# Performance work log

Hardware: AMD Instinct MI355X
Metric: run time of the kernel (lower is better)

The kernel has to match this reference:

```python
import jax, jax.numpy as jnp
import numpy as np

B, NQ, NV = 4, 16384, 16384
DIM, FRAMES = 64, 4
D = DIM * FRAMES            # embed_dims = 256
HEADS, POINTS, LEVELS = 8, 4, 1
HD = D // HEADS             # head_dim = 32
HL, WL = 128, 128           # single-level feature map, HL*WL == NV
EPS = 1e-6


def setup_inputs() -> dict:
    key = jax.random.key(0)
    ks = jax.random.split(key, 14)
    inp = {
        "query": jax.random.normal(ks[0], (B, NQ, D), jnp.float32),
        "feat": jax.random.normal(ks[1], (B, NV, D), jnp.float32),
        "reference_points": jax.random.uniform(ks[2], (B, NQ, LEVELS, 2), jnp.float32),
        "spatial_shapes": jnp.array([[HL, WL]], jnp.int32),
        "level_start_index": jnp.array([0], jnp.int32),
        # LayerNorm params
        "qn_scale": jnp.ones((D,), jnp.float32),
        "qn_bias": jnp.zeros((D,), jnp.float32),
        "fn_scale": jnp.ones((D,), jnp.float32),
        "fn_bias": jnp.zeros((D,), jnp.float32),
        # MSDeformAttn projections
        "W_value": jax.random.normal(ks[3], (D, D), jnp.float32) / np.sqrt(D),
        "b_value": jnp.zeros((D,), jnp.float32),
        "W_off": jax.random.normal(ks[4], (D, HEADS * LEVELS * POINTS * 2), jnp.float32) * 0.01,
        "b_off": jax.random.normal(ks[5], (HEADS * LEVELS * POINTS * 2,), jnp.float32) * 0.5,
        "W_attn": jax.random.normal(ks[6], (D, HEADS * LEVELS * POINTS), jnp.float32) * 0.02,
        "b_attn": jnp.zeros((HEADS * LEVELS * POINTS,), jnp.float32),
        "W_out": jax.random.normal(ks[7], (D, D), jnp.float32) / np.sqrt(D),
        "b_out": jnp.zeros((D,), jnp.float32),
        # gamma is a learned scale (init 0 in the module; randomized here so it contributes)
        "gamma": jax.random.normal(ks[8], (D,), jnp.float32) * 0.1,
    }
    return inp


def _layer_norm(x, scale, bias):
    mu = jnp.mean(x, axis=-1, keepdims=True)
    var = jnp.mean(jnp.square(x - mu), axis=-1, keepdims=True)
    return (x - mu) * jax.lax.rsqrt(var + EPS) * scale + bias


def _bilinear_gather(v, loc, Hl, Wl):
    # v:   [B, H, N, hd] flattened level values (row-major HxW)
    # loc: [B, H, NQ, P, 2] normalized sampling locations in [0,1]
    # grid_sample semantics: align_corners=False, zero padding
    x = loc[..., 0] * Wl - 0.5
    y = loc[..., 1] * Hl - 0.5
    x0 = jnp.floor(x); y0 = jnp.floor(y)
    x1 = x0 + 1.0;     y1 = y0 + 1.0
    wx1 = x - x0; wx0 = 1.0 - wx1
    wy1 = y - y0; wy0 = 1.0 - wy1
    out = 0.0
    for xi, yi, w in ((x0, y0, wx0 * wy0), (x1, y0, wx1 * wy0),
                      (x0, y1, wx0 * wy1), (x1, y1, wx1 * wy1)):
        inb = (xi >= 0) & (xi < Wl) & (yi >= 0) & (yi < Hl)
        idx = (jnp.clip(yi, 0, Hl - 1) * Wl + jnp.clip(xi, 0, Wl - 1)).astype(jnp.int32)
        Bc, Hc, NQc, Pc = idx.shape
        g = jnp.take_along_axis(v, idx.reshape(Bc, Hc, NQc * Pc)[..., None], axis=2)
        g = g.reshape(Bc, Hc, NQc, Pc, -1)          # [B, H, NQ, P, hd]
        out = out + g * (w * inb)[..., None]
    return out


def reference(query, feat, reference_points, spatial_shapes, level_start_index,
              qn_scale, qn_bias, fn_scale, fn_bias,
              W_value, b_value, W_off, b_off, W_attn, b_attn, W_out, b_out, gamma):
    Bq, nq, _ = query.shape
    q = _layer_norm(query, qn_scale, qn_bias)
    v = _layer_norm(feat, fn_scale, fn_bias)

    # value projection -> per-head values [B, H, NV, hd]
    value = (v @ W_value + b_value).reshape(Bq, -1, HEADS, HD).transpose(0, 2, 1, 3)

    # sampling offsets [B, NQ, H, L, P, 2] and attention weights (softmax over L*P)
    off = (q @ W_off + b_off).reshape(Bq, nq, HEADS, LEVELS, POINTS, 2)
    aw = jax.nn.softmax((q @ W_attn + b_attn).reshape(Bq, nq, HEADS, LEVELS * POINTS), axis=-1)
    aw = aw.reshape(Bq, nq, HEADS, LEVELS, POINTS)

    ss = np.asarray(spatial_shapes)          # static level geometry
    lsi = np.asarray(level_start_index)
    offset_norm = ss[:, ::-1].astype(np.float32)  # (W, H) per level
    # sampling locations [B, NQ, H, L, P, 2]
    loc = reference_points[:, :, None, :, None, :] + off / offset_norm[None, None, None, :, None, :]

    acc = jnp.zeros((Bq, HEADS, nq, HD), query.dtype)
    for l in range(LEVELS):
        Hl, Wl = int(ss[l, 0]), int(ss[l, 1])
        start = int(lsi[l])
        v_l = value[:, :, start:start + Hl * Wl]                # [B, H, Hl*Wl, hd]
        loc_l = loc[:, :, :, l].transpose(0, 2, 1, 3, 4)        # [B, H, NQ, P, 2]
        sampled = _bilinear_gather(v_l, loc_l, Hl, Wl)          # [B, H, NQ, P, hd]
        aw_l = aw[:, :, :, l].transpose(0, 2, 1, 3)             # [B, H, NQ, P]
        acc = acc + jnp.einsum('bhnpd,bhnp->bhnd', sampled, aw_l)

    out = acc.transpose(0, 2, 1, 3).reshape(Bq, nq, D) @ W_out + b_out
    return query + gamma * out
```

## Files before the change

kernel.cpp:

```cpp
#include <hip/hip_runtime.h>

#define NQ 16384
#define NV 16384
#define DMODEL 256

typedef __bf16 bf16x8 __attribute__((ext_vector_type(8)));
typedef float f32x4 __attribute__((ext_vector_type(4)));

__device__ __forceinline__ unsigned short f2bf(float x) {
    union { float f; unsigned int u; } v; v.f = x;
    unsigned int r = v.u + 0x7fff + ((v.u >> 16) & 1);
    return (unsigned short)(r >> 16);
}
__device__ __forceinline__ float blo(unsigned int u) {
    union { unsigned int u; float f; } v; v.u = u << 16; return v.f;
}
__device__ __forceinline__ float bhi(unsigned int u) {
    union { unsigned int u; float f; } v; v.u = u & 0xFFFF0000u; return v.f;
}
__device__ __forceinline__ f32x4 mfma16(bf16x8 a, bf16x8 b, f32x4 c) {
    return __builtin_amdgcn_mfma_f32_16x16x32_bf16(a, b, c, 0, 0, 0);
}

__global__ __launch_bounds__(256) void k_prep_ln(
    const float* __restrict__ Wv, const float* __restrict__ Woff,
    const float* __restrict__ Wattn, const float* __restrict__ Wout,
    unsigned short* __restrict__ WtV, unsigned short* __restrict__ WtC,
    unsigned short* __restrict__ WtO,
    const float* __restrict__ feat, const float* __restrict__ query,
    const float* __restrict__ fns, const float* __restrict__ fnb,
    const float* __restrict__ qns, const float* __restrict__ qnb,
    unsigned short* __restrict__ lnf, unsigned short* __restrict__ lnq) {
    if (blockIdx.x < 608) {
        int t = blockIdx.x * 256 + threadIdx.x;
        if (t < 256 * 256) { int n = t >> 8, k = t & 255; WtV[t] = f2bf(Wv[k * 256 + n]); return; }
        t -= 256 * 256;
        if (t < 256 * 256) { int n = t >> 8, k = t & 255; WtO[t] = f2bf(Wout[k * 256 + n]); return; }
        t -= 256 * 256;
        if (t < 96 * 256) {
            int j = t >> 8, k = t & 255;
            float w = (j < 64) ? Woff[k * 64 + j] : Wattn[k * 32 + (j - 64)];
            WtC[j * 256 + k] = f2bf(w);
        }
        return;
    }
    const int lb = blockIdx.x - 608;
    const float* src; const float* scale; const float* bias; unsigned short* dst;
    int row0;
    if (lb < 512) { src = feat;  scale = fns; bias = fnb; dst = lnf; row0 = lb * 128; }
    else          { src = query; scale = qns; bias = qnb; dst = lnq; row0 = (lb - 512) * 128; }
    const int lane = threadIdx.x & 63;
    const int w = threadIdx.x >> 6;
    const int g = lane >> 4, li = lane & 15;
    float4 sc[4], bi[4];
#pragma unroll
    for (int j = 0; j < 4; ++j) {
        sc[j] = *(const float4*)(scale + li * 16 + j * 4);
        bi[j] = *(const float4*)(bias + li * 16 + j * 4);
    }
    const int rbase = row0 + w * 8 + g;

    float4 xa[2][4], xb[2][4];
#define LN_LOAD(buf, coff)                                                            \
    _Pragma("unroll") for (int h2 = 0; h2 < 2; ++h2)                                  \
        _Pragma("unroll") for (int j = 0; j < 4; ++j)                                 \
            buf[h2][j] = *(const float4*)(src + (size_t)(rbase + (coff) + h2 * 4) * 256 + li * 16 + j * 4);
#define LN_PROC(buf, coff)                                                            \
    _Pragma("unroll") for (int h2 = 0; h2 < 2; ++h2) {                                \
        float s = 0.f, sq = 0.f;                                                      \
        _Pragma("unroll") for (int j = 0; j < 4; ++j) {                               \
            s  += buf[h2][j].x + buf[h2][j].y + buf[h2][j].z + buf[h2][j].w;          \
            sq += buf[h2][j].x * buf[h2][j].x + buf[h2][j].y * buf[h2][j].y +         \
                  buf[h2][j].z * buf[h2][j].z + buf[h2][j].w * buf[h2][j].w;          \
        }                                                                             \
        _Pragma("unroll") for (int d = 1; d < 16; d <<= 1) {                          \
            s  += __shfl_xor(s, d);                                                   \
            sq += __shfl_xor(sq, d);                                                  \
        }                                                                             \
        float mu = s * 0.00390625f;                                                   \
        float rstd = rsqrtf(sq * 0.00390625f - mu * mu + 1e-6f);                      \
        unsigned int pk[8];                                                           \
        _Pragma("unroll") for (int j = 0; j < 4; ++j) {                               \
            pk[2 * j] = (unsigned)f2bf((buf[h2][j].x - mu) * rstd * sc[j].x + bi[j].x) |      \
                        ((unsigned)f2bf((buf[h2][j].y - mu) * rstd * sc[j].y + bi[j].y) << 16); \
            pk[2 * j + 1] = (unsigned)f2bf((buf[h2][j].z - mu) * rstd * sc[j].z + bi[j].z) |   \
                            ((unsigned)f2bf((buf[h2][j].w - mu) * rstd * sc[j].w + bi[j].w) << 16); \
        }                                                                             \
        uint4* dstp = (uint4*)(dst + (size_t)(rbase + (coff) + h2 * 4) * 256 + li * 16); \
        dstp[0] = make_uint4(pk[0], pk[1], pk[2], pk[3]);                             \
        dstp[1] = make_uint4(pk[4], pk[5], pk[6], pk[7]);                             \
    }
    LN_LOAD(xa, 0)
    LN_LOAD(xb, 32)
    LN_PROC(xa, 0)
    LN_LOAD(xa, 64)
    LN_PROC(xb, 32)
    LN_LOAD(xb, 96)
    LN_PROC(xa, 64)
    LN_PROC(xb, 96)
}

#define STAGE_A(srcbuf)                                                               \
    {                                                                                 \
        const int c = threadIdx.x & 31;                                               \
        const int rt = threadIdx.x >> 5;                                              \
        _Pragma("unroll") for (int i = 0; i < 16; ++i) {                              \
            const int r = rt + i * 8;                                                 \
            *(uint4*)&A[r * 264 + c * 8] =                                            \
                *(const uint4*)((srcbuf) + (size_t)(m0 + r) * 256 + c * 8);           \
        }                                                                             \
    }

#define MFMA_STEP_V(bf, kk)                                                           \
    _Pragma("unroll") for (int m = 0; m < 8; ++m) {                                   \
        bf16x8 a = *(const bf16x8*)&A[(m * 16 + lrow) * 264 + (kk) * 32 + lk];        \
        _Pragma("unroll") for (int i = 0; i < 4; ++i)                                 \
            acc[i][m] = mfma16(bf[i], a, acc[i][m]);                                  \
    }

__global__ __launch_bounds__(256) void k_value(
    const unsigned short* __restrict__ lnf, const float* __restrict__ b_value,
    const unsigned short* __restrict__ WtV, unsigned short* __restrict__ value) {
    __shared__ unsigned short A[128 * 264];
    const int m0 = blockIdx.x * 128;
    STAGE_A(lnf)
    __syncthreads();
    const int lane = threadIdx.x & 63;
    const int w = threadIdx.x >> 6;
    const int lrow = lane & 15, lk = (lane >> 4) * 8;
    f32x4 acc[4][8];
#pragma unroll
    for (int i = 0; i < 4; ++i)
#pragma unroll
        for (int m = 0; m < 8; ++m) acc[i][m] = (f32x4){0.f, 0.f, 0.f, 0.f};
#define LOADB_V(dst, kk)                                                              \
    _Pragma("unroll") for (int i = 0; i < 4; ++i) dst[i] =                            \
        *(const bf16x8*)(WtV + (size_t)((w * 4 + i) * 16 + lrow) * 256 + (kk) * 32 + lk);
    {
        bf16x8 b0[4], b1[4];
        LOADB_V(b0, 0)
#pragma unroll
        for (int k2 = 0; k2 < 4; ++k2) {
            LOADB_V(b1, k2 * 2 + 1)
            MFMA_STEP_V(b0, k2 * 2)
            if (k2 < 3) { LOADB_V(b0, k2 * 2 + 2) }
            MFMA_STEP_V(b1, k2 * 2 + 1)
        }
    }
    __syncthreads();
    const int g = lane >> 4;
#pragma unroll
    for (int i = 0; i < 4; ++i) {
        const int col0 = (w * 4 + i) * 16 + g * 4;
        float4 bv = *(const float4*)(b_value + col0);
#pragma unroll
        for (int m = 0; m < 8; ++m) {
            uint2 r;
            r.x = (unsigned)f2bf(acc[i][m][0] + bv.x) | ((unsigned)f2bf(acc[i][m][1] + bv.y) << 16);
            r.y = (unsigned)f2bf(acc[i][m][2] + bv.z) | ((unsigned)f2bf(acc[i][m][3] + bv.w) << 16);
            *(uint2*)&A[(m * 16 + (lane & 15)) * 264 + col0] = r;
        }
    }
    __syncthreads();
    {
        const int c = threadIdx.x & 31;
        const int rt = threadIdx.x >> 5;
#pragma unroll
        for (int i = 0; i < 16; ++i) {
            const int r = rt + i * 8;
            *(uint4*)(value + (size_t)(m0 + r) * 256 + c * 8) = *(uint4*)&A[r * 264 + c * 8];
        }
    }
}

__global__ __launch_bounds__(256) void k_qoff(
    const unsigned short* __restrict__ lnq, const float* __restrict__ refpt,
    const float* __restrict__ b_off, const float* __restrict__ b_attn,
    const unsigned short* __restrict__ WtC, float4* __restrict__ samples) {
    __shared__ unsigned short A[128 * 264];
    const int m0 = blockIdx.x * 128;
    STAGE_A(lnq)
    __syncthreads();
    const int lane = threadIdx.x & 63;
    const int w = threadIdx.x >> 6;
    const int lrow = lane & 15, lk = (lane >> 4) * 8;
    f32x4 acc[6][2];
#pragma unroll
    for (int i = 0; i < 6; ++i)
#pragma unroll
        for (int m = 0; m < 2; ++m) acc[i][m] = (f32x4){0.f, 0.f, 0.f, 0.f};
#define LOADB_Q(dst, kk)                                                              \
    _Pragma("unroll") for (int i = 0; i < 6; ++i) dst[i] =                            \
        *(const bf16x8*)(WtC + (size_t)(i * 16 + lrow) * 256 + (kk) * 32 + lk);
#define MFMA_STEP_Q(bf, kk)                                                           \
    _Pragma("unroll") for (int m = 0; m < 2; ++m) {                                   \
        bf16x8 a = *(const bf16x8*)&A[(w * 32 + m * 16 + lrow) * 264 + (kk) * 32 + lk]; \
        _Pragma("unroll") for (int i = 0; i < 6; ++i)                                 \
            acc[i][m] = mfma16(bf[i], a, acc[i][m]);                                  \
    }
    {
        bf16x8 b0[6], b1[6];
        LOADB_Q(b0, 0)
#pragma unroll
        for (int k2 = 0; k2 < 4; ++k2) {
            LOADB_Q(b1, k2 * 2 + 1)
            MFMA_STEP_Q(b0, k2 * 2)
            if (k2 < 3) { LOADB_Q(b0, k2 * 2 + 2) }
            MFMA_STEP_Q(b1, k2 * 2 + 1)
        }
    }
    __syncthreads();
    float* Dl = (float*)A + w * 4224;
#pragma unroll
    for (int i = 0; i < 6; ++i) {
        const int col0 = i * 16 + (lane >> 4) * 4;
#pragma unroll
        for (int m = 0; m < 2; ++m) {
            const int rl = m * 16 + (lane & 15);
            *(float4*)&Dl[rl * 100 + col0] =
                make_float4(acc[i][m][0], acc[i][m][1], acc[i][m][2], acc[i][m][3]);
        }
    }
    __syncthreads();
#pragma unroll
    for (int it = 0; it < 4; ++it) {
        int idx = it * 64 + lane;
        int rl = idx >> 3;
        int h = idx & 7;
        int row = m0 + w * 32 + rl;
        float rx = refpt[(size_t)row * 2 + 0] * 128.f - 0.5f;
        float ry = refpt[(size_t)row * 2 + 1] * 128.f - 0.5f;
        float l0 = Dl[rl * 100 + 64 + h * 4 + 0] + b_attn[h * 4 + 0];
        float l1 = Dl[rl * 100 + 64 + h * 4 + 1] + b_attn[h * 4 + 1];
        float l2 = Dl[rl * 100 + 64 + h * 4 + 2] + b_attn[h * 4 + 2];
        float l3 = Dl[rl * 100 + 64 + h * 4 + 3] + b_attn[h * 4 + 3];
        float mx = fmaxf(fmaxf(l0, l1), fmaxf(l2, l3));
        float e0 = __expf(l0 - mx), e1 = __expf(l1 - mx);
        float e2 = __expf(l2 - mx), e3 = __expf(l3 - mx);
        float inv = 1.f / (e0 + e1 + e2 + e3);
        float ww[4] = {e0 * inv, e1 * inv, e2 * inv, e3 * inv};
#pragma unroll
        for (int p = 0; p < 4; ++p) {
            float ox = Dl[rl * 100 + h * 8 + p * 2 + 0] + b_off[h * 8 + p * 2 + 0];
            float oy = Dl[rl * 100 + h * 8 + p * 2 + 1] + b_off[h * 8 + p * 2 + 1];
            samples[((size_t)row * 8 + h) * 4 + p] = make_float4(rx + ox, ry + oy, ww[p], 0.f);
        }
    }
}

__global__ __launch_bounds__(256) void k_gather(
    const unsigned short* __restrict__ value, const float4* __restrict__ samples,
    unsigned short* __restrict__ accb) {
    const int tid = blockIdx.x * 256 + threadIdx.x;
    const int sub = tid & 3;
    const int t = tid >> 2;
    const int h = t & 7;
    const int bq = t >> 3;
    const int b = bq >> 14;
    const unsigned short* vb = value + ((size_t)b << 14) * 256 + h * 32 + sub * 8;
    float a0 = 0.f, a1 = 0.f, a2 = 0.f, a3 = 0.f;
    float a4 = 0.f, a5 = 0.f, a6 = 0.f, a7 = 0.f;
#pragma unroll
    for (int p = 0; p < 4; ++p) {
        float4 s = samples[(size_t)t * 4 + p];
        float xf = floorf(s.x), yf = floorf(s.y);
        float fx = s.x - xf, fy = s.y - yf;
        int x0 = (int)xf, y0 = (int)yf;
        int x1 = x0 + 1, y1 = y0 + 1;
        float wgt = s.z;
        bool bx0 = (unsigned)x0 < 128u, bx1 = (unsigned)x1 < 128u;
        bool by0 = (unsigned)y0 < 128u, by1 = (unsigned)y1 < 128u;
        float wt[4];
        wt[0] = (bx0 && by0) ? (1.f - fx) * (1.f - fy) * wgt : 0.f;
        wt[1] = (bx1 && by0) ? fx * (1.f - fy) * wgt : 0.f;
        wt[2] = (bx0 && by1) ? (1.f - fx) * fy * wgt : 0.f;
        wt[3] = (bx1 && by1) ? fx * fy * wgt : 0.f;
        int xc0 = min(max(x0, 0), 127), xc1 = min(max(x1, 0), 127);
        int yc0 = min(max(y0, 0), 127), yc1 = min(max(y1, 0), 127);
        int pix[4];
        pix[0] = yc0 * 128 + xc0; pix[1] = yc0 * 128 + xc1;
        pix[2] = yc1 * 128 + xc0; pix[3] = yc1 * 128 + xc1;
#pragma unroll
        for (int tp = 0; tp < 4; ++tp) {
            uint4 u = *(const uint4*)(vb + (size_t)pix[tp] * 256);
            float w = wt[tp];
            a0 = fmaf(w, blo(u.x), a0); a1 = fmaf(w, bhi(u.x), a1);
            a2 = fmaf(w, blo(u.y), a2); a3 = fmaf(w, bhi(u.y), a3);
            a4 = fmaf(w, blo(u.z), a4); a5 = fmaf(w, bhi(u.z), a5);
            a6 = fmaf(w, blo(u.w), a6); a7 = fmaf(w, bhi(u.w), a7);
        }
    }
    uint4 r;
    r.x = (unsigned)f2bf(a0) | ((unsigned)f2bf(a1) << 16);
    r.y = (unsigned)f2bf(a2) | ((unsigned)f2bf(a3) << 16);
    r.z = (unsigned)f2bf(a4) | ((unsigned)f2bf(a5) << 16);
    r.w = (unsigned)f2bf(a6) | ((unsigned)f2bf(a7) << 16);
    *(uint4*)(accb + (size_t)bq * 256 + h * 32 + sub * 8) = r;
}

__global__ __launch_bounds__(256) void k_out(
    const unsigned short* __restrict__ accb, const unsigned short* __restrict__ WtO,
    const float* __restrict__ b_out, const float* __restrict__ gamma,
    const float* __restrict__ query, float* __restrict__ out) {
    __shared__ unsigned short A[128 * 264];
    const int m0 = blockIdx.x * 128;
    STAGE_A(accb)
    __syncthreads();
    const int lane = threadIdx.x & 63;
    const int w = threadIdx.x >> 6;
    const int lrow = lane & 15, lk = (lane >> 4) * 8;
    f32x4 acc[4][8];
#pragma unroll
    for (int i = 0; i < 4; ++i)
#pragma unroll
        for (int m = 0; m < 8; ++m) acc[i][m] = (f32x4){0.f, 0.f, 0.f, 0.f};
#define LOADB_O(dst, kk)                                                              \
    _Pragma("unroll") for (int i = 0; i < 4; ++i) dst[i] =                            \
        *(const bf16x8*)(WtO + (size_t)((w * 4 + i) * 16 + lrow) * 256 + (kk) * 32 + lk);
    {
        bf16x8 b0[4], b1[4];
        LOADB_O(b0, 0)
#pragma unroll
        for (int k2 = 0; k2 < 4; ++k2) {
            LOADB_O(b1, k2 * 2 + 1)
            MFMA_STEP_V(b0, k2 * 2)
            if (k2 < 3) { LOADB_O(b0, k2 * 2 + 2) }
            MFMA_STEP_V(b1, k2 * 2 + 1)
        }
    }
    const int g = lane >> 4;
    float4 bo[4], gm[4];
#pragma unroll
    for (int i = 0; i < 4; ++i) {
        bo[i] = *(const float4*)(b_out + (w * 4 + i) * 16 + g * 4);
        gm[i] = *(const float4*)(gamma + (w * 4 + i) * 16 + g * 4);
    }
#pragma unroll
    for (int m = 0; m < 8; ++m) {
        const size_t row = (size_t)(m0 + m * 16 + (lane & 15));
#pragma unroll
        for (int i = 0; i < 4; ++i) {
            const int col0 = (w * 4 + i) * 16 + g * 4;
            float4 q = *(const float4*)(query + row * 256 + col0);
            float4 o;
            o.x = q.x + gm[i].x * (acc[i][m][0] + bo[i].x);
            o.y = q.y + gm[i].y * (acc[i][m][1] + bo[i].y);
            o.z = q.z + gm[i].z * (acc[i][m][2] + bo[i].z);
            o.w = q.w + gm[i].w * (acc[i][m][3] + bo[i].w);
            *(float4*)(out + row * 256 + col0) = o;
        }
    }
}

extern "C" void kernel_launch(void* const* d_in, const int* in_sizes, int n_in,
                              void* d_out, int out_size, void* d_ws, size_t ws_size,
                              hipStream_t stream) {
    const float* query    = (const float*)d_in[0];
    const float* feat     = (const float*)d_in[1];
    const float* refpt    = (const float*)d_in[2];
    const float* qn_scale = (const float*)d_in[5];
    const float* qn_bias  = (const float*)d_in[6];
    const float* fn_scale = (const float*)d_in[7];
    const float* fn_bias  = (const float*)d_in[8];
    const float* W_value  = (const float*)d_in[9];
    const float* b_value  = (const float*)d_in[10];
    const float* W_off    = (const float*)d_in[11];
    const float* b_off    = (const float*)d_in[12];
    const float* W_attn   = (const float*)d_in[13];
    const float* b_attn   = (const float*)d_in[14];
    const float* W_out    = (const float*)d_in[15];
    const float* b_out    = (const float*)d_in[16];
    const float* gamma    = (const float*)d_in[17];
    float* out = (float*)d_out;

    char* ws = (char*)d_ws;
    unsigned short* WtV   = (unsigned short*)(ws);
    unsigned short* WtO   = (unsigned short*)(ws + 131072);
    unsigned short* WtC   = (unsigned short*)(ws + 262144);
    unsigned short* value = (unsigned short*)(ws + 311296);
    char* regA = ws + 311296 + 33554432;
    char* regB = ws + 311296 + 2 * 33554432;
    unsigned short* lnf     = (unsigned short*)regA;
    float4*         samples = (float4*)regA;
    unsigned short* lnq     = (unsigned short*)regB;
    unsigned short* accb    = (unsigned short*)regB;

    hipLaunchKernelGGL(k_prep_ln, dim3(1632), dim3(256), 0, stream,
                       W_value, W_off, W_attn, W_out, WtV, WtC, WtO,
                       feat, query, fn_scale, fn_bias, qn_scale, qn_bias, lnf, lnq);
    hipLaunchKernelGGL(k_value, dim3(512), dim3(256), 0, stream,
                       lnf, b_value, WtV, value);
    hipLaunchKernelGGL(k_qoff, dim3(512), dim3(256), 0, stream,
                       lnq, refpt, b_off, b_attn, WtC, samples);
    hipLaunchKernelGGL(k_gather, dim3(8192), dim3(256), 0, stream,
                       value, samples, accb);
    hipLaunchKernelGGL(k_out, dim3(512), dim3(256), 0, stream,
                       accb, WtO, b_out, gamma, query, out);
}
```

Measured before the change: 191.4 us.

## Fold LayerNorm into projection GEMMs via precomputed weight column sums

Removes the separate LayerNorm pass that wrote normalized bf16 copies of feat and query. The raw inputs are now converted to bf16 in the GEMM staging step, which also computes per-row mean and rstd. LayerNorm scale is folded into the weights, and the bias and mean terms are applied algebraically in the epilogue using precomputed column sums. This saves one full read and write of both 64 MB inputs. The cost is precision: raw un-normalized values are rounded to bf16 and then have a large mean term subtracted after the GEMM, and the staging step uses a less coalesced per-thread load pattern.

New measurement: 175.6 us. 8.2% less time.

```diff
diff --git a/kernel.cpp b/kernel.cpp
--- a/kernel.cpp
+++ b/kernel.cpp
@@ -22,83 +22,99 @@
     return __builtin_amdgcn_mfma_f32_16x16x32_bf16(a, b, c, 0, 0, 0);
 }
 
-__global__ __launch_bounds__(256) void k_prep_ln(
+__global__ __launch_bounds__(256) void k_prep(
     const float* __restrict__ Wv, const float* __restrict__ Woff,
     const float* __restrict__ Wattn, const float* __restrict__ Wout,
+    const float* __restrict__ fns, const float* __restrict__ fnb,
+    const float* __restrict__ qns, const float* __restrict__ qnb,
+    const float* __restrict__ b_value, const float* __restrict__ b_off,
+    const float* __restrict__ b_attn,
     unsigned short* __restrict__ WtV, unsigned short* __restrict__ WtC,
     unsigned short* __restrict__ WtO,
-    const float* __restrict__ feat, const float* __restrict__ query,
-    const float* __restrict__ fns, const float* __restrict__ fnb,
-    const float* __restrict__ qns, const float* __restrict__ qnb,
-    unsigned short* __restrict__ lnf, unsigned short* __restrict__ lnq) {
-    if (blockIdx.x < 608) {
-        int t = blockIdx.x * 256 + threadIdx.x;
-        if (t < 256 * 256) { int n = t >> 8, k = t & 255; WtV[t] = f2bf(Wv[k * 256 + n]); return; }
-        t -= 256 * 256;
-        if (t < 256 * 256) { int n = t >> 8, k = t & 255; WtO[t] = f2bf(Wout[k * 256 + n]); return; }
-        t -= 256 * 256;
-        if (t < 96 * 256) {
+    float* __restrict__ csumV, float* __restrict__ preV,
+    float* __restrict__ csumC, float* __restrict__ preC) {
+    const int blk = blockIdx.x;
+    if (blk < 608) {
+        int t = blk * 256 + threadIdx.x;
+        if (t < 65536) { int n = t >> 8, k = t & 255; WtV[t] = f2bf(fns[k] * Wv[k * 256 + n]); return; }
+        t -= 65536;
+        if (t < 65536) { int n = t >> 8, k = t & 255; WtO[t] = f2bf(Wout[k * 256 + n]); return; }
+        t -= 65536;
+        if (t < 24576) {
             int j = t >> 8, k = t & 255;
             float w = (j < 64) ? Woff[k * 64 + j] : Wattn[k * 32 + (j - 64)];
-            WtC[j * 256 + k] = f2bf(w);
+            WtC[j * 256 + k] = f2bf(qns[k] * w);
         }
         return;
     }
-    const int lb = blockIdx.x - 608;
-    const float* src; const float* scale; const float* bias; unsigned short* dst;
-    int row0;
-    if (lb < 512) { src = feat;  scale = fns; bias = fnb; dst = lnf; row0 = lb * 128; }
-    else          { src = query; scale = qns; bias = qnb; dst = lnq; row0 = (lb - 512) * 128; }
-    const int lane = threadIdx.x & 63;
-    const int w = threadIdx.x >> 6;
-    const int g = lane >> 4, li = lane & 15;
-    float4 sc[4], bi[4];
-#pragma unroll
-    for (int j = 0; j < 4; ++j) {
-        sc[j] = *(const float4*)(scale + li * 16 + j * 4);
-        bi[j] = *(const float4*)(bias + li * 16 + j * 4);
-    }
-    const int rbase = row0 + w * 8 + g;
-
-    float4 xa[2][4], xb[2][4];
-#define LN_LOAD(buf, coff)                                                            \
-    _Pragma("unroll") for (int h2 = 0; h2 < 2; ++h2)                                  \
-        _Pragma("unroll") for (int j = 0; j < 4; ++j)                                 \
-            buf[h2][j] = *(const float4*)(src + (size_t)(rbase + (coff) + h2 * 4) * 256 + li * 16 + j * 4);
-#define LN_PROC(buf, coff)                                                            \
-    _Pragma("unroll") for (int h2 = 0; h2 < 2; ++h2) {                                \
+    if (blk < 612) {
+        __shared__ float sCS[4][64], sPR[4][64];
+        const int nl = threadIdx.x & 63;
+        const int n = (blk - 608) * 64 + nl;
+        const int kp = threadIdx.x >> 6;
+        float cs = 0.f, pr = 0.f;
+        for (int k = kp * 64; k < kp * 64 + 64; ++k) {
+            float w = Wv[k * 256 + n];
+            cs += fns[k] * w;
+            pr += fnb[k] * w;
+        }
+        sCS[kp][nl] = cs; sPR[kp][nl] = pr;
+        __syncthreads();
+        if (threadIdx.x < 64) {
+            int nn = (blk - 608) * 64 + threadIdx.x;
+            csumV[nn] = sCS[0][threadIdx.x] + sCS[1][threadIdx.x] + sCS[2][threadIdx.x] + sCS[3][threadIdx.x];
+            preV[nn] = sPR[0][threadIdx.x] + sPR[1][threadIdx.x] + sPR[2][threadIdx.x] + sPR[3][threadIdx.x]
+                       + b_value[nn];
+        }
+        return;
+    }
+    {
+        __shared__ float sCS[2][96], sPR[2][96];
+        const int t = threadIdx.x;
+        if (t < 192) {
+            const int n = t % 96;
+            const int kp = t / 96;
+            float cs = 0.f, pr = 0.f;
+            for (int k = kp * 128; k < kp * 128 + 128; ++k) {
+                float w = (n < 64) ? Woff[k * 64 + n] : Wattn[k * 32 + (n - 64)];
+                cs += qns[k] * w;
+                pr += qnb[k] * w;
+            }
+            sCS[kp][n] = cs; sPR[kp][n] = pr;
+        }
+        __syncthreads();
+        if (t < 96) {
+            csumC[t] = sCS[0][t] + sCS[1][t];
+            preC[t] = sPR[0][t] + sPR[1][t] + ((t < 64) ? b_off[t] : b_attn[t - 64]);
+        }
+        return;
+    }
+}
+
+#define STAGE_RAW(srcptr)                                                             \
+    {                                                                                 \
+        const int t = threadIdx.x;                                                    \
+        const int r = t >> 1, h = t & 1;                                              \
+        const float* src = (srcptr) + (size_t)(m0 + r) * 256 + h * 128;               \
+        unsigned short* dstp = &A[r * 264 + h * 128];                                 \
         float s = 0.f, sq = 0.f;                                                      \
-        _Pragma("unroll") for (int j = 0; j < 4; ++j) {                               \
-            s  += buf[h2][j].x + buf[h2][j].y + buf[h2][j].z + buf[h2][j].w;          \
-            sq += buf[h2][j].x * buf[h2][j].x + buf[h2][j].y * buf[h2][j].y +         \
-                  buf[h2][j].z * buf[h2][j].z + buf[h2][j].w * buf[h2][j].w;          \
+        _Pragma("unroll 8") for (int j = 0; j < 32; ++j) {                            \
+            float4 x = *(const float4*)(src + j * 4);                                 \
+            s += x.x + x.y + x.z + x.w;                                               \
+            sq += x.x * x.x + x.y * x.y + x.z * x.z + x.w * x.w;                      \
+            uint2 pk;                                                                 \
+            pk.x = (unsigned)f2bf(x.x) | ((unsigned)f2bf(x.y) << 16);                 \
+            pk.y = (unsigned)f2bf(x.z) | ((unsigned)f2bf(x.w) << 16);                 \
+            *(uint2*)(dstp + j * 4) = pk;                                             \
         }                                                                             \
-        _Pragma("unroll") for (int d = 1; d < 16; d <<= 1) {                          \
-            s  += __shfl_xor(s, d);                                                   \
-            sq += __shfl_xor(sq, d);                                                  \
+        s += __shfl_xor(s, 1);                                                        \
+        sq += __shfl_xor(sq, 1);                                                      \
+        if (h == 0) {                                                                 \
+            float mu = s * 0.00390625f;                                               \
+            muL[r] = mu;                                                              \
+            rsL[r] = rsqrtf(sq * 0.00390625f - mu * mu + 1e-6f);                      \
         }                                                                             \
-        float mu = s * 0.00390625f;                                                   \
-        float rstd = rsqrtf(sq * 0.00390625f - mu * mu + 1e-6f);                      \
-        unsigned int pk[8];                                                           \
-        _Pragma("unroll") for (int j = 0; j < 4; ++j) {                               \
-            pk[2 * j] = (unsigned)f2bf((buf[h2][j].x - mu) * rstd * sc[j].x + bi[j].x) |      \
-                        ((unsigned)f2bf((buf[h2][j].y - mu) * rstd * sc[j].y + bi[j].y) << 16); \
-            pk[2 * j + 1] = (unsigned)f2bf((buf[h2][j].z - mu) * rstd * sc[j].z + bi[j].z) |   \
-                            ((unsigned)f2bf((buf[h2][j].w - mu) * rstd * sc[j].w + bi[j].w) << 16); \
-        }                                                                             \
-        uint4* dstp = (uint4*)(dst + (size_t)(rbase + (coff) + h2 * 4) * 256 + li * 16); \
-        dstp[0] = make_uint4(pk[0], pk[1], pk[2], pk[3]);                             \
-        dstp[1] = make_uint4(pk[4], pk[5], pk[6], pk[7]);                             \
-    }
-    LN_LOAD(xa, 0)
-    LN_LOAD(xb, 32)
-    LN_PROC(xa, 0)
-    LN_LOAD(xa, 64)
-    LN_PROC(xb, 32)
-    LN_LOAD(xb, 96)
-    LN_PROC(xa, 64)
-    LN_PROC(xb, 96)
-}
+    }
 
 #define STAGE_A(srcbuf)                                                               \
     {                                                                                 \
@@ -119,11 +135,13 @@
     }
 
 __global__ __launch_bounds__(256) void k_value(
-    const unsigned short* __restrict__ lnf, const float* __restrict__ b_value,
-    const unsigned short* __restrict__ WtV, unsigned short* __restrict__ value) {
+    const float* __restrict__ feat, const float* __restrict__ csumV,
+    const float* __restrict__ preV, const unsigned short* __restrict__ WtV,
+    unsigned short* __restrict__ value) {
     __shared__ unsigned short A[128 * 264];
+    __shared__ float muL[128], rsL[128];
     const int m0 = blockIdx.x * 128;
-    STAGE_A(lnf)
+    STAGE_RAW(feat)
     __syncthreads();
     const int lane = threadIdx.x & 63;
     const int w = threadIdx.x >> 6;
@@ -152,13 +170,18 @@
 #pragma unroll
     for (int i = 0; i < 4; ++i) {
         const int col0 = (w * 4 + i) * 16 + g * 4;
-        float4 bv = *(const float4*)(b_value + col0);
+        float4 cs = *(const float4*)(csumV + col0);
+        float4 pr = *(const float4*)(preV + col0);
 #pragma unroll
         for (int m = 0; m < 8; ++m) {
+            const int rl = m * 16 + (lane & 15);
+            float mu = muL[rl], rs = rsL[rl];
             uint2 r;
-            r.x = (unsigned)f2bf(acc[i][m][0] + bv.x) | ((unsigned)f2bf(acc[i][m][1] + bv.y) << 16);
-            r.y = (unsigned)f2bf(acc[i][m][2] + bv.z) | ((unsigned)f2bf(acc[i][m][3] + bv.w) << 16);
-            *(uint2*)&A[(m * 16 + (lane & 15)) * 264 + col0] = r;
+            r.x = (unsigned)f2bf(rs * (acc[i][m][0] - mu * cs.x) + pr.x) |
+                  ((unsigned)f2bf(rs * (acc[i][m][1] - mu * cs.y) + pr.y) << 16);
+            r.y = (unsigned)f2bf(rs * (acc[i][m][2] - mu * cs.z) + pr.z) |
+                  ((unsigned)f2bf(rs * (acc[i][m][3] - mu * cs.w) + pr.w) << 16);
+            *(uint2*)&A[rl * 264 + col0] = r;
         }
     }
     __syncthreads();
@@ -174,12 +197,13 @@
 }
 
 __global__ __launch_bounds__(256) void k_qoff(
-    const unsigned short* __restrict__ lnq, const float* __restrict__ refpt,
-    const float* __restrict__ b_off, const float* __restrict__ b_attn,
+    const float* __restrict__ query, const float* __restrict__ refpt,
+    const float* __restrict__ csumC, const float* __restrict__ preC,
     const unsigned short* __restrict__ WtC, float4* __restrict__ samples) {
     __shared__ unsigned short A[128 * 264];
+    __shared__ float muL[128], rsL[128];
     const int m0 = blockIdx.x * 128;
-    STAGE_A(lnq)
+    STAGE_RAW(query)
     __syncthreads();
     const int lane = threadIdx.x & 63;
     const int w = threadIdx.x >> 6;
@@ -228,12 +252,13 @@
         int rl = idx >> 3;
         int h = idx & 7;
         int row = m0 + w * 32 + rl;
+        float mu = muL[w * 32 + rl], rs = rsL[w * 32 + rl];
         float rx = refpt[(size_t)row * 2 + 0] * 128.f - 0.5f;
         float ry = refpt[(size_t)row * 2 + 1] * 128.f - 0.5f;
-        float l0 = Dl[rl * 100 + 64 + h * 4 + 0] + b_attn[h * 4 + 0];
-        float l1 = Dl[rl * 100 + 64 + h * 4 + 1] + b_attn[h * 4 + 1];
-        float l2 = Dl[rl * 100 + 64 + h * 4 + 2] + b_attn[h * 4 + 2];
-        float l3 = Dl[rl * 100 + 64 + h * 4 + 3] + b_attn[h * 4 + 3];
+        float l0 = rs * (Dl[rl * 100 + 64 + h * 4 + 0] - mu * csumC[64 + h * 4 + 0]) + preC[64 + h * 4 + 0];
+        float l1 = rs * (Dl[rl * 100 + 64 + h * 4 + 1] - mu * csumC[64 + h * 4 + 1]) + preC[64 + h * 4 + 1];
+        float l2 = rs * (Dl[rl * 100 + 64 + h * 4 + 2] - mu * csumC[64 + h * 4 + 2]) + preC[64 + h * 4 + 2];
+        float l3 = rs * (Dl[rl * 100 + 64 + h * 4 + 3] - mu * csumC[64 + h * 4 + 3]) + preC[64 + h * 4 + 3];
         float mx = fmaxf(fmaxf(l0, l1), fmaxf(l2, l3));
         float e0 = __expf(l0 - mx), e1 = __expf(l1 - mx);
         float e2 = __expf(l2 - mx), e3 = __expf(l3 - mx);
@@ -241,8 +266,8 @@
         float ww[4] = {e0 * inv, e1 * inv, e2 * inv, e3 * inv};
 #pragma unroll
         for (int p = 0; p < 4; ++p) {
-            float ox = Dl[rl * 100 + h * 8 + p * 2 + 0] + b_off[h * 8 + p * 2 + 0];
-            float oy = Dl[rl * 100 + h * 8 + p * 2 + 1] + b_off[h * 8 + p * 2 + 1];
+            float ox = rs * (Dl[rl * 100 + h * 8 + p * 2 + 0] - mu * csumC[h * 8 + p * 2 + 0]) + preC[h * 8 + p * 2 + 0];
+            float oy = rs * (Dl[rl * 100 + h * 8 + p * 2 + 1] - mu * csumC[h * 8 + p * 2 + 1]) + preC[h * 8 + p * 2 + 1];
             samples[((size_t)row * 8 + h) * 4 + p] = make_float4(rx + ox, ry + oy, ww[p], 0.f);
         }
     }
@@ -377,21 +402,23 @@
     unsigned short* WtV   = (unsigned short*)(ws);
     unsigned short* WtO   = (unsigned short*)(ws + 131072);
     unsigned short* WtC   = (unsigned short*)(ws + 262144);
-    unsigned short* value = (unsigned short*)(ws + 311296);
-    char* regA = ws + 311296 + 33554432;
-    char* regB = ws + 311296 + 2 * 33554432;
-    unsigned short* lnf     = (unsigned short*)regA;
-    float4*         samples = (float4*)regA;
-    unsigned short* lnq     = (unsigned short*)regB;
-    unsigned short* accb    = (unsigned short*)regB;
-
-    hipLaunchKernelGGL(k_prep_ln, dim3(1632), dim3(256), 0, stream,
-                       W_value, W_off, W_attn, W_out, WtV, WtC, WtO,
-                       feat, query, fn_scale, fn_bias, qn_scale, qn_bias, lnf, lnq);
+    float* csumV = (float*)(ws + 311296);
+    float* preV  = (float*)(ws + 312320);
+    float* csumC = (float*)(ws + 313344);
+    float* preC  = (float*)(ws + 313856);
+    unsigned short* value = (unsigned short*)(ws + 315392);
+    float4* samples       = (float4*)(ws + 315392 + 33554432);
+    unsigned short* accb  = (unsigned short*)(ws + 315392 + 2 * 33554432);
+
+    hipLaunchKernelGGL(k_prep, dim3(613), dim3(256), 0, stream,
+                       W_value, W_off, W_attn, W_out,
+                       fn_scale, fn_bias, qn_scale, qn_bias,
+                       b_value, b_off, b_attn,
+                       WtV, WtC, WtO, csumV, preV, csumC, preC);
     hipLaunchKernelGGL(k_value, dim3(512), dim3(256), 0, stream,
-                       lnf, b_value, WtV, value);
+                       feat, csumV, preV, WtV, value);
     hipLaunchKernelGGL(k_qoff, dim3(512), dim3(256), 0, stream,
-                       lnq, refpt, b_off, b_attn, WtC, samples);
+                       query, refpt, csumC, preC, WtC, samples);
     hipLaunchKernelGGL(k_gather, dim3(8192), dim3(256), 0, stream,
                        value, samples, accb);
     hipLaunchKernelGGL(k_out, dim3(512), dim3(256), 0, stream,
```
